# Kernel optimization log

Measured on AMD Instinct MI355X. Metric: run time of the kernel, lower is better.

## Reference

```python
import jax, jax.numpy as jnp
import numpy as np

N = 100000      # nodes
E = 1600000     # edges (before self loops)
F_IN = 128
HID = 32
H = 4
OUT = 32
NEG_SLOPE = 0.2


def setup_inputs() -> dict:
    key = jax.random.key(0)
    ks = jax.random.split(key, 10)
    x = jax.random.normal(ks[0], (N, F_IN), jnp.float32)
    edge_index = jax.random.randint(ks[1], (2, E), 0, N, jnp.int32)
    s1 = 1.0 / np.sqrt(F_IN)
    s2 = 1.0 / np.sqrt(H * HID)
    W1 = jax.random.normal(ks[2], (F_IN, H * HID), jnp.float32) * s1
    a_src1 = jax.random.normal(ks[3], (H, HID), jnp.float32) * 0.1
    a_dst1 = jax.random.normal(ks[4], (H, HID), jnp.float32) * 0.1
    b1 = jnp.zeros((H * HID,), jnp.float32)
    W2 = jax.random.normal(ks[5], (H * HID, OUT), jnp.float32) * s2
    a_src2 = jax.random.normal(ks[6], (1, OUT), jnp.float32) * 0.1
    a_dst2 = jax.random.normal(ks[7], (1, OUT), jnp.float32) * 0.1
    b2 = jnp.zeros((OUT,), jnp.float32)
    return {"x": x, "edge_index": edge_index, "W1": W1, "a_src1": a_src1,
            "a_dst1": a_dst1, "b1": b1, "W2": W2, "a_src2": a_src2,
            "a_dst2": a_dst2, "b2": b2}


def gat_conv(x, src, dst, W, a_src, a_dst, b, heads, out_ch):
    # PyG GATConv (concat=True) with self loops already appended to src/dst.
    n = x.shape[0]
    h = (x @ W).reshape(n, heads, out_ch)                 # [N,H,C]
    alpha_s = jnp.sum(h * a_src, axis=-1)                 # [N,H]
    alpha_d = jnp.sum(h * a_dst, axis=-1)                 # [N,H]
    e = jax.nn.leaky_relu(alpha_s[src] + alpha_d[dst], NEG_SLOPE)  # [E',H]
    # segment softmax over destination nodes (self loops => every segment nonempty)
    emax = jax.ops.segment_max(e, dst, num_segments=n)
    ex = jnp.exp(e - emax[dst])
    denom = jax.ops.segment_sum(ex, dst, num_segments=n)
    alpha = ex / denom[dst]                               # [E',H]
    msg = h[src] * alpha[:, :, None]                      # [E',H,C]
    out = jax.ops.segment_sum(msg, dst, num_segments=n)   # [N,H,C]
    return out.reshape(n, heads * out_ch) + b


def reference(x, edge_index, W1, a_src1, a_dst1, b1, W2, a_src2, a_dst2, b2):
    loops = jnp.arange(N, dtype=edge_index.dtype)
    src = jnp.concatenate([edge_index[0], loops])
    dst = jnp.concatenate([edge_index[1], loops])
    h = gat_conv(x, src, dst, W1, a_src1, a_dst1, b1, H, HID)
    h = jax.nn.relu(h)                                    # dropout: eval mode, no-op
    out = gat_conv(h, src, dst, W2, a_src2, a_dst2, b2, 1, OUT)
    return out
```

## Files before the change

kernel.cpp:

```cpp
#include <hip/hip_runtime.h>
#include <hip/hip_fp16.h>

#define NEG 0.2f
#define EPB 4096
#define BSH 6
#define SLOT 48
#define CAP 1280
#define KBMAX 1664

typedef _Float16 half8 __attribute__((ext_vector_type(8)));
typedef float f32x4 __attribute__((ext_vector_type(4)));

__device__ inline __half2 pun_h2(float f) { union { float f; __half2 h; } u; u.f = f; return u.h; }
__device__ inline float pun_f(__half2 h) { union { float f; __half2 h; } u; u.h = h; return u.f; }

__global__ void k_prep(const float* __restrict__ W1, const float* __restrict__ W2,
                       half8* __restrict__ Wp, half8* __restrict__ W2p,
                       int* __restrict__ gcount, int KB) {
    int b = blockIdx.x;
    if (b < 8) {
        int u = b * 256 + threadIdx.x;
        int s = u >> 9, tn = (u >> 6) & 7, lane = u & 63;
        int quad = lane >> 4, c = lane & 15;
        half8 v;
#pragma unroll
        for (int j = 0; j < 8; ++j)
            v[j] = (_Float16)W1[(s * 32 + quad * 8 + j) * 128 + tn * 16 + c];
        Wp[u] = v;
    } else if (b < 10) {
        int u = (b - 8) * 256 + threadIdx.x;
        int n = u >> 8, s = (u >> 6) & 3, lane = u & 63;
        int quad = lane >> 4, c = lane & 15;
        half8 v;
#pragma unroll
        for (int j = 0; j < 8; ++j)
            v[j] = (_Float16)W2[(s * 32 + quad * 8 + j) * 32 + n * 16 + c];
        W2p[u] = v;
    } else {
        int i = (b - 10) * 256 + threadIdx.x;
        if (i < KB) gcount[i] = 0;
    }
}

__global__ __launch_bounds__(256) void k_pA(const float* __restrict__ x,
                                            const half8* __restrict__ Wp,
                                            const float* __restrict__ a_s,
                                            const float* __restrict__ a_d,
                                            __half* __restrict__ h1h,
                                            float* __restrict__ as1,
                                            float* __restrict__ ad1, int N,
                                            const int* __restrict__ srcp,
                                            const int* __restrict__ dstp,
                                            int* __restrict__ gcount,
                                            int2* __restrict__ ebuf,
                                            int E, int KB, int ngemm) {
    __shared__ _Float16 xa[64][136];
    __shared__ int lh[KBMAX];
    int t = threadIdx.x;

    if (blockIdx.x >= ngemm) {
        int blk = blockIdx.x - ngemm;
        int base0 = blk * EPB;
        int ss[16], dd[16];
#pragma unroll
        for (int j = 0; j < 16; ++j) {
            int i = base0 + j * 256 + t;
            if (i < E) { ss[j] = srcp[i]; dd[j] = dstp[i]; } else dd[j] = -1;
        }
        for (int i = t; i < KB; i += 256) lh[i] = 0;
        __syncthreads();
#pragma unroll
        for (int j = 0; j < 16; ++j)
            if (dd[j] >= 0) atomicAdd(&lh[dd[j] >> BSH], 1);
        __syncthreads();
        for (int b = t; b < KB; b += 256) {
            int c = lh[b];
            if (c > 0) lh[b] = atomicAdd(&gcount[b], c);
        }
        __syncthreads();
#pragma unroll
        for (int j = 0; j < 16; ++j) {
            if (dd[j] >= 0) {
                int b = dd[j] >> BSH;
                int pos = atomicAdd(&lh[b], 1);
                ebuf[(size_t)b * CAP + pos] = int2{ss[j], dd[j]};
            }
        }
        return;
    }

    int row0 = blockIdx.x * 64;
    {
        int row = t >> 2;
        int col0 = (t & 3) * 32;
        int gr = row0 + row;
        const float4* xsrc = (const float4*)&x[(size_t)gr * 128 + col0];
#pragma unroll
        for (int m = 0; m < 4; ++m) {
            float4 p0, p1;
            if (gr < N) { p0 = xsrc[m * 2]; p1 = xsrc[m * 2 + 1]; }
            else { p0 = float4{0,0,0,0}; p1 = float4{0,0,0,0}; }
            _Float16* dstq = &xa[row][col0 + m * 8];
            dstq[0] = (_Float16)p0.x; dstq[1] = (_Float16)p0.y;
            dstq[2] = (_Float16)p0.z; dstq[3] = (_Float16)p0.w;
            dstq[4] = (_Float16)p1.x; dstq[5] = (_Float16)p1.y;
            dstq[6] = (_Float16)p1.z; dstq[7] = (_Float16)p1.w;
        }
    }
    __syncthreads();

    int w = t >> 6;
    int lane = t & 63;
    int quad = lane >> 4, c = lane & 15;

    f32x4 acc[8];
#pragma unroll
    for (int i = 0; i < 8; ++i) acc[i] = f32x4{0, 0, 0, 0};

#pragma unroll
    for (int s = 0; s < 4; ++s) {
        half8 a = *(const half8*)&xa[w * 16 + c][s * 32 + quad * 8];
#pragma unroll
        for (int tn = 0; tn < 8; ++tn) {
            half8 b = Wp[(s * 8 + tn) * 64 + lane];
            acc[tn] = __builtin_amdgcn_mfma_f32_16x16x32_f16(a, b, acc[tn], 0, 0, 0);
        }
    }

    float asv[8], adv[8];
#pragma unroll
    for (int tn = 0; tn < 8; ++tn) { asv[tn] = a_s[tn * 16 + c]; adv[tn] = a_d[tn * 16 + c]; }
#pragma unroll
    for (int r = 0; r < 4; ++r) {
        int gr = row0 + w * 16 + quad * 4 + r;
#pragma unroll
        for (int h = 0; h < 4; ++h) {
            float ps = acc[2*h][r] * asv[2*h] + acc[2*h+1][r] * asv[2*h+1];
            float pd = acc[2*h][r] * adv[2*h] + acc[2*h+1][r] * adv[2*h+1];
            ps += __shfl_xor(ps, 1); ps += __shfl_xor(ps, 2);
            ps += __shfl_xor(ps, 4); ps += __shfl_xor(ps, 8);
            pd += __shfl_xor(pd, 1); pd += __shfl_xor(pd, 2);
            pd += __shfl_xor(pd, 4); pd += __shfl_xor(pd, 8);
            if (c == 0 && gr < N) { as1[gr * 4 + h] = ps; ad1[gr * 4 + h] = pd; }
        }
    }

    __syncthreads();
#pragma unroll
    for (int tn = 0; tn < 8; ++tn)
#pragma unroll
        for (int r = 0; r < 4; ++r)
            xa[w * 16 + quad * 4 + r][tn * 16 + c] = (_Float16)acc[tn][r];
    __syncthreads();
    {
        int row = t >> 2;
        int seg = t & 3;
        int gr = row0 + row;
        if (gr < N) {
            float4* gp = (float4*)&h1h[(size_t)gr * 128 + seg * 32];
#pragma unroll
            for (int i = 0; i < 4; ++i)
                gp[i] = *(float4*)&xa[row][seg * 32 + i * 8];
        }
    }
}

__global__ __launch_bounds__(256) void k_aggC(const int2* __restrict__ ebuf,
                                              const int* __restrict__ gcount,
                                              const __half* __restrict__ h1h,
                                              const float* __restrict__ as1,
                                              const float* __restrict__ ad1,
                                              const float* __restrict__ b1,
                                              const half8* __restrict__ W2p,
                                              const float* __restrict__ asw,
                                              const float* __restrict__ adw,
                                              int* __restrict__ csr,
                                              int* __restrict__ counts,
                                              __half* __restrict__ h2h,
                                              float* __restrict__ as2,
                                              float* __restrict__ ad2, int N) {
    __shared__ int lcnt[64];
    __shared__ int lcsr[64 * SLOT];
    __shared__ _Float16 stg[4][16][136];
    int t = threadIdx.x;
    int b = blockIdx.x, d0 = b << BSH;

    if (t < 64) lcnt[t] = 0;
    __syncthreads();

    int ecnt = gcount[b];
    const int2* eb = &ebuf[(size_t)b * CAP];
    for (int i = t; i < ecnt; i += 256) {
        int2 e = eb[i];
        int li = e.y - d0;
        int r = atomicAdd(&lcnt[li], 1);
        lcsr[li * SLOT + r] = e.x;
    }
    __syncthreads();

    {
        int4* gc = (int4*)&csr[(size_t)d0 * SLOT];
        const int4* lc = (const int4*)lcsr;
#pragma unroll
        for (int u = 0; u < 3; ++u) gc[t + 256 * u] = lc[t + 256 * u];
        if (t < 64 && d0 + t < N) counts[d0 + t] = lcnt[t];
    }

    int w = t >> 6, lane = t & 63;
    int q = lane >> 5, c4 = lane & 31;
    int head4 = c4 >> 3;
    const __half2* hp = (const __half2*)h1h;
    float4 bv4 = *(const float4*)&b1[4 * c4];

    int quad = lane >> 4, c16 = lane & 15;
    half8 bf[2][4];
#pragma unroll
    for (int n = 0; n < 2; ++n)
#pragma unroll
        for (int s = 0; s < 4; ++s) bf[n][s] = W2p[(n * 4 + s) * 64 + lane];
    float asw0 = asw[c16], asw1 = asw[16 + c16];
    float adw0 = adw[c16], adw1 = adw[16 + c16];

    for (int i = 0; i < 16; ++i) {
        int dst = d0 + w * 16 + i;
        bool valid = dst < N;
        int li = w * 16 + i;
        int cnt = valid ? lcnt[li] : 0;
        int cbase = li * SLOT;
        float adv = valid ? ad1[dst * 4 + head4] : 0.f;
        float a0 = 0.f, a1 = 0.f, a2 = 0.f, a3 = 0.f, den = 0.f;
        if (valid && q == 0) {
            float es = as1[dst * 4 + head4] + adv;
            es = es > 0.f ? es : NEG * es;
            float xs = __expf(es);
            float2 vv = *(const float2*)&hp[(size_t)dst * 64 + 2 * c4];
            float2 f01 = __half22float2(pun_h2(vv.x));
            float2 f23 = __half22float2(pun_h2(vv.y));
            a0 = xs * f01.x; a1 = xs * f01.y; a2 = xs * f23.x; a3 = xs * f23.y;
            den = xs;
        }
        int e = q;
        for (; e + 14 < cnt; e += 16) {
            int si[8];
#pragma unroll
            for (int j = 0; j < 8; ++j) si[j] = lcsr[cbase + e + 2 * j];
            float ej[8];
#pragma unroll
            for (int j = 0; j < 8; ++j) ej[j] = as1[si[j] * 4 + head4];
            float2 vj[8];
#pragma unroll
            for (int j = 0; j < 8; ++j) vj[j] = *(const float2*)&hp[(size_t)si[j] * 64 + 2 * c4];
#pragma unroll
            for (int j = 0; j < 8; ++j) {
                float ee = ej[j] + adv;
                ee = ee > 0.f ? ee : NEG * ee;
                float xw = __expf(ee);
                float2 f01 = __half22float2(pun_h2(vj[j].x));
                float2 f23 = __half22float2(pun_h2(vj[j].y));
                a0 += xw * f01.x; a1 += xw * f01.y;
                a2 += xw * f23.x; a3 += xw * f23.y;
                den += xw;
            }
        }
        for (; e + 6 < cnt; e += 8) {
            int si[4];
#pragma unroll
            for (int j = 0; j < 4; ++j) si[j] = lcsr[cbase + e + 2 * j];
            float ej[4];
#pragma unroll
            for (int j = 0; j < 4; ++j) ej[j] = as1[si[j] * 4 + head4];
            float2 vj[4];
#pragma unroll
            for (int j = 0; j < 4; ++j) vj[j] = *(const float2*)&hp[(size_t)si[j] * 64 + 2 * c4];
#pragma unroll
            for (int j = 0; j < 4; ++j) {
                float ee = ej[j] + adv;
                ee = ee > 0.f ? ee : NEG * ee;
                float xw = __expf(ee);
                float2 f01 = __half22float2(pun_h2(vj[j].x));
                float2 f23 = __half22float2(pun_h2(vj[j].y));
                a0 += xw * f01.x; a1 += xw * f01.y;
                a2 += xw * f23.x; a3 += xw * f23.y;
                den += xw;
            }
        }
        for (; e < cnt; e += 2) {
            int s0 = lcsr[cbase + e];
            float e0v = as1[s0 * 4 + head4] + adv;
            float2 vv = *(const float2*)&hp[(size_t)s0 * 64 + 2 * c4];
            e0v = e0v > 0.f ? e0v : NEG * e0v;  float x0 = __expf(e0v);
            float2 f01 = __half22float2(pun_h2(vv.x));
            float2 f23 = __half22float2(pun_h2(vv.y));
            a0 += x0 * f01.x; a1 += x0 * f01.y;
            a2 += x0 * f23.x; a3 += x0 * f23.y;
            den += x0;
        }
        a0 += __shfl_xor(a0, 32); a1 += __shfl_xor(a1, 32);
        a2 += __shfl_xor(a2, 32); a3 += __shfl_xor(a3, 32);
        den += __shfl_xor(den, 32);
        float inv = valid ? 1.f / den : 0.f;
        float o0 = a0 * inv + bv4.x;
        float o1 = a1 * inv + bv4.y;
        float o2 = a2 * inv + bv4.z;
        float o3 = a3 * inv + bv4.w;
        o0 = o0 > 0.f ? o0 : 0.f;
        o1 = o1 > 0.f ? o1 : 0.f;
        o2 = o2 > 0.f ? o2 : 0.f;
        o3 = o3 > 0.f ? o3 : 0.f;
        if (q == 0) {
            float2 st;
            st.x = pun_f(__floats2half2_rn(o0, o1));
            st.y = pun_f(__floats2half2_rn(o2, o3));
            *(float2*)&stg[w][i][4 * c4] = st;
        }
    }

    f32x4 am0 = {0, 0, 0, 0}, am1 = {0, 0, 0, 0};
#pragma unroll
    for (int s = 0; s < 4; ++s) {
        half8 a = *(const half8*)&stg[w][c16][s * 32 + quad * 8];
        am0 = __builtin_amdgcn_mfma_f32_16x16x32_f16(a, bf[0][s], am0, 0, 0, 0);
        am1 = __builtin_amdgcn_mfma_f32_16x16x32_f16(a, bf[1][s], am1, 0, 0, 0);
    }
#pragma unroll
    for (int r = 0; r < 4; ++r) {
        int dst = d0 + w * 16 + quad * 4 + r;
        float ps = am0[r] * asw0 + am1[r] * asw1;
        float pd = am0[r] * adw0 + am1[r] * adw1;
        ps += __shfl_xor(ps, 1); ps += __shfl_xor(ps, 2);
        ps += __shfl_xor(ps, 4); ps += __shfl_xor(ps, 8);
        pd += __shfl_xor(pd, 1); pd += __shfl_xor(pd, 2);
        pd += __shfl_xor(pd, 4); pd += __shfl_xor(pd, 8);
        if (dst < N) {
            h2h[(size_t)dst * 32 + c16]      = __float2half_rn(am0[r]);
            h2h[(size_t)dst * 32 + 16 + c16] = __float2half_rn(am1[r]);
            if (c16 == 0) { as2[dst] = ps; ad2[dst] = pd; }
        }
    }
}

__global__ __launch_bounds__(256) void k_agg2(const __half* __restrict__ h2h,
                                              const float* __restrict__ as2,
                                              const float* __restrict__ ad2,
                                              const int* __restrict__ csr,
                                              const int* __restrict__ counts,
                                              const float* __restrict__ b2,
                                              float* __restrict__ out, int N) {
    int w = threadIdx.x >> 6;
    int lane = threadIdx.x & 63;
    int dst = blockIdx.x * 4 + w;
    if (dst >= N) return;
    int q = lane >> 5;
    int c = lane & 31;
    float adv = ad2[dst];
    int beg = dst * SLOT;
    int cnt = counts[dst];
    float acc = 0.f, den = 0.f;
    if (q == 0) {
        float es = as2[dst] + adv;
        es = es > 0.f ? es : NEG * es;
        float xs = __expf(es);
        acc = xs * __half2float(h2h[(size_t)dst * 32 + c]);
        den = xs;
    }
    int e = q;
    for (; e + 6 < cnt; e += 8) {
        int si[4];
#pragma unroll
        for (int j = 0; j < 4; ++j) si[j] = csr[beg + e + 2 * j];
        float ej[4];
#pragma unroll
        for (int j = 0; j < 4; ++j) ej[j] = as2[si[j]];
        float vj[4];
#pragma unroll
        for (int j = 0; j < 4; ++j) vj[j] = __half2float(h2h[(size_t)si[j] * 32 + c]);
#pragma unroll
        for (int j = 0; j < 4; ++j) {
            float ee = ej[j] + adv;
            ee = ee > 0.f ? ee : NEG * ee;
            float xw = __expf(ee);
            acc += xw * vj[j];
            den += xw;
        }
    }
    for (; e < cnt; e += 2) {
        int s0 = csr[beg + e];
        float e0 = as2[s0] + adv;
        float v0 = __half2float(h2h[(size_t)s0 * 32 + c]);
        e0 = e0 > 0.f ? e0 : NEG * e0;  float x0 = __expf(e0);
        acc += x0 * v0;
        den += x0;
    }
    acc += __shfl_xor(acc, 32, 64);
    den += __shfl_xor(den, 32, 64);
    if (q == 0) out[(size_t)dst * 32 + c] = acc / den + b2[c];
}

extern "C" void kernel_launch(void* const* d_in, const int* in_sizes, int n_in,
                              void* d_out, int out_size, void* d_ws, size_t ws_size,
                              hipStream_t stream) {
    const float* x     = (const float*)d_in[0];
    const int*   ei    = (const int*)d_in[1];
    const float* W1    = (const float*)d_in[2];
    const float* as_w1 = (const float*)d_in[3];
    const float* ad_w1 = (const float*)d_in[4];
    const float* b1    = (const float*)d_in[5];
    const float* W2    = (const float*)d_in[6];
    const float* as_w2 = (const float*)d_in[7];
    const float* ad_w2 = (const float*)d_in[8];
    const float* b2    = (const float*)d_in[9];
    float* out = (float*)d_out;

    int N  = in_sizes[0] / 128;
    int E  = in_sizes[1] / 2;
    const int* srcp = ei;
    const int* dstp = ei + E;

    int KB     = (N + 63) >> BSH;
    int ND     = KB << BSH;
    int nblkB  = (E + EPB - 1) / EPB;
    int ngemm  = (N + 63) / 64;

    char* p = (char*)d_ws;
    auto alloc = [&](size_t bytes) -> char* {
        char* r = p;
        p += (bytes + 255) & ~(size_t)255;
        return r;
    };
    __half* h1h    = (__half*)alloc((size_t)N * 128 * 2);
    float*  as1    = (float*)alloc((size_t)N * 4 * 4);
    float*  ad1    = (float*)alloc((size_t)N * 4 * 4);
    __half* h2h    = (__half*)alloc((size_t)N * 32 * 2);
    float*  as2    = (float*)alloc((size_t)N * 4);
    float*  ad2    = (float*)alloc((size_t)N * 4);
    int*    counts = (int*)alloc((size_t)ND * 4);
    int*    csr    = (int*)alloc((size_t)ND * SLOT * 4);
    half8*  Wp     = (half8*)alloc(2048 * 16);
    half8*  W2p    = (half8*)alloc(512 * 16);
    int*    gcount = (int*)alloc((size_t)KB * 4);
    int2*   ebuf   = (int2*)alloc((size_t)KB * CAP * 8);

    k_prep<<<10 + (KB + 255) / 256, 256, 0, stream>>>(W1, W2, Wp, W2p, gcount, KB);
    k_pA<<<ngemm + nblkB, 256, 0, stream>>>(x, Wp, as_w1, ad_w1, h1h, as1, ad1, N,
                                            srcp, dstp, gcount, ebuf, E, KB, ngemm);
    k_aggC<<<KB, 256, 0, stream>>>(ebuf, gcount, h1h, as1, ad1, b1,
                                   W2p, as_w2, ad_w2, csr, counts, h2h, as2, ad2, N);
    k_agg2<<<(N + 3) / 4, 256, 0, stream>>>(h2h, as2, ad2, csr, counts, b2, out, N);
}
```

Before: 291.8 us.

## Split aggC blocks into half-size 128-thread blocks and unroll agg2 gather deeper

Each 64-destination bucket is now handled by two 128-thread blocks that each scan the whole bucket edge list and keep only their 32 destinations. This halves LDS per block, adds a launch_bounds occupancy hint and defers the W2 fragment loads past the aggregation loop to reduce register pressure. In exchange every edge in a bucket is read twice. Separately, k_agg2 gains an 8-wide unrolled gather loop so more loads are in flight per iteration.

```diff
diff --git a/kernel.cpp b/kernel.cpp
--- a/kernel.cpp
+++ b/kernel.cpp
@@ -165,7 +165,7 @@
     }
 }
 
-__global__ __launch_bounds__(256) void k_aggC(const int2* __restrict__ ebuf,
+__global__ __launch_bounds__(128, 5) void k_aggC(const int2* __restrict__ ebuf,
                                               const int* __restrict__ gcount,
                                               const __half* __restrict__ h1h,
                                               const float* __restrict__ as1,
@@ -179,22 +179,26 @@
                                               __half* __restrict__ h2h,
                                               float* __restrict__ as2,
                                               float* __restrict__ ad2, int N) {
-    __shared__ int lcnt[64];
-    __shared__ int lcsr[64 * SLOT];
-    __shared__ _Float16 stg[4][16][136];
+    __shared__ int lcnt[32];
+    __shared__ int lcsr[32 * SLOT];
+    __shared__ _Float16 stg[2][16][136];
     int t = threadIdx.x;
-    int b = blockIdx.x, d0 = b << BSH;
-
-    if (t < 64) lcnt[t] = 0;
+    int b = blockIdx.x;
+    int bucket = b >> 1;
+    int d0 = b << 5;
+
+    if (t < 32) lcnt[t] = 0;
     __syncthreads();
 
-    int ecnt = gcount[b];
-    const int2* eb = &ebuf[(size_t)b * CAP];
-    for (int i = t; i < ecnt; i += 256) {
+    int ecnt = gcount[bucket];
+    const int2* eb = &ebuf[(size_t)bucket * CAP];
+    for (int i = t; i < ecnt; i += 128) {
         int2 e = eb[i];
-        int li = e.y - d0;
-        int r = atomicAdd(&lcnt[li], 1);
-        lcsr[li * SLOT + r] = e.x;
+        unsigned li = (unsigned)(e.y - d0);
+        if (li < 32u) {
+            int r = atomicAdd(&lcnt[li], 1);
+            lcsr[li * SLOT + r] = e.x;
+        }
     }
     __syncthreads();
 
@@ -202,8 +206,8 @@
         int4* gc = (int4*)&csr[(size_t)d0 * SLOT];
         const int4* lc = (const int4*)lcsr;
 #pragma unroll
-        for (int u = 0; u < 3; ++u) gc[t + 256 * u] = lc[t + 256 * u];
-        if (t < 64 && d0 + t < N) counts[d0 + t] = lcnt[t];
+        for (int u = 0; u < 3; ++u) gc[t + 128 * u] = lc[t + 128 * u];
+        if (t < 32 && d0 + t < N) counts[d0 + t] = lcnt[t];
     }
 
     int w = t >> 6, lane = t & 63;
@@ -211,15 +215,6 @@
     int head4 = c4 >> 3;
     const __half2* hp = (const __half2*)h1h;
     float4 bv4 = *(const float4*)&b1[4 * c4];
-
-    int quad = lane >> 4, c16 = lane & 15;
-    half8 bf[2][4];
-#pragma unroll
-    for (int n = 0; n < 2; ++n)
-#pragma unroll
-        for (int s = 0; s < 4; ++s) bf[n][s] = W2p[(n * 4 + s) * 64 + lane];
-    float asw0 = asw[c16], asw1 = asw[16 + c16];
-    float adw0 = adw[c16], adw1 = adw[16 + c16];
 
     for (int i = 0; i < 16; ++i) {
         int dst = d0 + w * 16 + i;
@@ -314,6 +309,15 @@
             *(float2*)&stg[w][i][4 * c4] = st;
         }
     }
+
+    int quad = lane >> 4, c16 = lane & 15;
+    half8 bf[2][4];
+#pragma unroll
+    for (int n = 0; n < 2; ++n)
+#pragma unroll
+        for (int s = 0; s < 4; ++s) bf[n][s] = W2p[(n * 4 + s) * 64 + lane];
+    float asw0 = asw[c16], asw1 = asw[16 + c16];
+    float adw0 = adw[c16], adw1 = adw[16 + c16];
 
     f32x4 am0 = {0, 0, 0, 0}, am1 = {0, 0, 0, 0};
 #pragma unroll
@@ -364,6 +368,25 @@
         den = xs;
     }
     int e = q;
+    for (; e + 14 < cnt; e += 16) {
+        int si[8];
+#pragma unroll
+        for (int j = 0; j < 8; ++j) si[j] = csr[beg + e + 2 * j];
+        float ej[8];
+#pragma unroll
+        for (int j = 0; j < 8; ++j) ej[j] = as2[si[j]];
+        float vj[8];
+#pragma unroll
+        for (int j = 0; j < 8; ++j) vj[j] = __half2float(h2h[(size_t)si[j] * 32 + c]);
+#pragma unroll
+        for (int j = 0; j < 8; ++j) {
+            float ee = ej[j] + adv;
+            ee = ee > 0.f ? ee : NEG * ee;
+            float xw = __expf(ee);
+            acc += xw * vj[j];
+            den += xw;
+        }
+    }
     for (; e + 6 < cnt; e += 8) {
         int si[4];
 #pragma unroll
@@ -443,7 +466,7 @@
     k_prep<<<10 + (KB + 255) / 256, 256, 0, stream>>>(W1, W2, Wp, W2p, gcount, KB);
     k_pA<<<ngemm + nblkB, 256, 0, stream>>>(x, Wp, as_w1, ad_w1, h1h, as1, ad1, N,
                                             srcp, dstp, gcount, ebuf, E, KB, ngemm);
-    k_aggC<<<KB, 256, 0, stream>>>(ebuf, gcount, h1h, as1, ad1, b1,
-                                   W2p, as_w2, ad_w2, csr, counts, h2h, as2, ad2, N);
+    k_aggC<<<KB * 2, 128, 0, stream>>>(ebuf, gcount, h1h, as1, ad1, b1,
+                                       W2p, as_w2, ad_w2, csr, counts, h2h, as2, ad2, N);
     k_agg2<<<(N + 3) / 4, 256, 0, stream>>>(h2h, as2, ad2, csr, counts, b2, out, N);
 }
```

After: 298.4 us. 2.3% more time.

## Aggregate layer 2 directly from bucketed edge buffer with LDS atomics, drop CSR

Applied to the files above, without the earlier changes.

k_aggC no longer writes the padded CSR and count arrays to global memory. k_agg2 now runs one block per 64-destination bucket, reads the unsorted ebuf edges directly and accumulates the softmax numerator and denominator into shared-memory arrays with atomics. The self-loop term is added in the epilogue. This removes the CSR global write and reread, and the per-node launch of 4 destinations per block, at the cost of LDS atomic contention and fewer, larger blocks. The W2 fragment loads are also moved later in k_aggC to shorten their register live range.

```diff
diff --git a/kernel.cpp b/kernel.cpp
--- a/kernel.cpp
+++ b/kernel.cpp
@@ -174,8 +174,6 @@
                                               const half8* __restrict__ W2p,
                                               const float* __restrict__ asw,
                                               const float* __restrict__ adw,
-                                              int* __restrict__ csr,
-                                              int* __restrict__ counts,
                                               __half* __restrict__ h2h,
                                               float* __restrict__ as2,
                                               float* __restrict__ ad2, int N) {
@@ -198,28 +196,11 @@
     }
     __syncthreads();
 
-    {
-        int4* gc = (int4*)&csr[(size_t)d0 * SLOT];
-        const int4* lc = (const int4*)lcsr;
-#pragma unroll
-        for (int u = 0; u < 3; ++u) gc[t + 256 * u] = lc[t + 256 * u];
-        if (t < 64 && d0 + t < N) counts[d0 + t] = lcnt[t];
-    }
-
     int w = t >> 6, lane = t & 63;
     int q = lane >> 5, c4 = lane & 31;
     int head4 = c4 >> 3;
     const __half2* hp = (const __half2*)h1h;
     float4 bv4 = *(const float4*)&b1[4 * c4];
-
-    int quad = lane >> 4, c16 = lane & 15;
-    half8 bf[2][4];
-#pragma unroll
-    for (int n = 0; n < 2; ++n)
-#pragma unroll
-        for (int s = 0; s < 4; ++s) bf[n][s] = W2p[(n * 4 + s) * 64 + lane];
-    float asw0 = asw[c16], asw1 = asw[16 + c16];
-    float adw0 = adw[c16], adw1 = adw[16 + c16];
 
     for (int i = 0; i < 16; ++i) {
         int dst = d0 + w * 16 + i;
@@ -315,6 +296,15 @@
         }
     }
 
+    int quad = lane >> 4, c16 = lane & 15;
+    half8 bf[2][4];
+#pragma unroll
+    for (int n = 0; n < 2; ++n)
+#pragma unroll
+        for (int s = 0; s < 4; ++s) bf[n][s] = W2p[(n * 4 + s) * 64 + lane];
+    float asw0 = asw[c16], asw1 = asw[16 + c16];
+    float adw0 = adw[c16], adw1 = adw[16 + c16];
+
     f32x4 am0 = {0, 0, 0, 0}, am1 = {0, 0, 0, 0};
 #pragma unroll
     for (int s = 0; s < 4; ++s) {
@@ -339,61 +329,68 @@
     }
 }
 
-__global__ __launch_bounds__(256) void k_agg2(const __half* __restrict__ h2h,
+__global__ __launch_bounds__(256) void k_agg2(const int2* __restrict__ ebuf,
+                                              const int* __restrict__ gcount,
+                                              const __half* __restrict__ h2h,
                                               const float* __restrict__ as2,
                                               const float* __restrict__ ad2,
-                                              const int* __restrict__ csr,
-                                              const int* __restrict__ counts,
                                               const float* __restrict__ b2,
                                               float* __restrict__ out, int N) {
-    int w = threadIdx.x >> 6;
-    int lane = threadIdx.x & 63;
-    int dst = blockIdx.x * 4 + w;
-    if (dst >= N) return;
-    int q = lane >> 5;
-    int c = lane & 31;
-    float adv = ad2[dst];
-    int beg = dst * SLOT;
-    int cnt = counts[dst];
-    float acc = 0.f, den = 0.f;
-    if (q == 0) {
-        float es = as2[dst] + adv;
+    __shared__ float acc[64][32];
+    __shared__ float den[64];
+    __shared__ float lad[64];
+    int t = threadIdx.x;
+    int b = blockIdx.x, d0 = b << BSH;
+
+    for (int u = t; u < 64 * 32; u += 256) ((float*)acc)[u] = 0.f;
+    if (t < 64) {
+        den[t] = 0.f;
+        lad[t] = (d0 + t < N) ? ad2[d0 + t] : 0.f;
+    }
+    __syncthreads();
+
+    int hw = t >> 5;
+    int c  = t & 31;
+    int ecnt = gcount[b];
+    const int2* eb = &ebuf[(size_t)b * CAP];
+
+    for (int base = hw * 8; base < ecnt; base += 64) {
+        int2 ed[8];
+#pragma unroll
+        for (int j = 0; j < 8; ++j)
+            if (base + j < ecnt) ed[j] = eb[base + j];
+        float asv[8];
+#pragma unroll
+        for (int j = 0; j < 8; ++j)
+            if (base + j < ecnt) asv[j] = as2[ed[j].x];
+        __half hv[8];
+#pragma unroll
+        for (int j = 0; j < 8; ++j)
+            if (base + j < ecnt) hv[j] = h2h[(size_t)ed[j].x * 32 + c];
+#pragma unroll
+        for (int j = 0; j < 8; ++j) {
+            if (base + j < ecnt) {
+                int li = ed[j].y - d0;
+                float ee = asv[j] + lad[li];
+                ee = ee > 0.f ? ee : NEG * ee;
+                float xw = __expf(ee);
+                atomicAdd(&acc[li][c], xw * __half2float(hv[j]));
+                if (c == 0) atomicAdd(&den[li], xw);
+            }
+        }
+    }
+    __syncthreads();
+
+    for (int u = t; u < 64 * 32; u += 256) {
+        int li = u >> 5, cc = u & 31;
+        int dst = d0 + li;
+        if (dst >= N) continue;
+        float es = as2[dst] + lad[li];
         es = es > 0.f ? es : NEG * es;
         float xs = __expf(es);
-        acc = xs * __half2float(h2h[(size_t)dst * 32 + c]);
-        den = xs;
-    }
-    int e = q;
-    for (; e + 6 < cnt; e += 8) {
-        int si[4];
-#pragma unroll
-        for (int j = 0; j < 4; ++j) si[j] = csr[beg + e + 2 * j];
-        float ej[4];
-#pragma unroll
-        for (int j = 0; j < 4; ++j) ej[j] = as2[si[j]];
-        float vj[4];
-#pragma unroll
-        for (int j = 0; j < 4; ++j) vj[j] = __half2float(h2h[(size_t)si[j] * 32 + c]);
-#pragma unroll
-        for (int j = 0; j < 4; ++j) {
-            float ee = ej[j] + adv;
-            ee = ee > 0.f ? ee : NEG * ee;
-            float xw = __expf(ee);
-            acc += xw * vj[j];
-            den += xw;
-        }
-    }
-    for (; e < cnt; e += 2) {
-        int s0 = csr[beg + e];
-        float e0 = as2[s0] + adv;
-        float v0 = __half2float(h2h[(size_t)s0 * 32 + c]);
-        e0 = e0 > 0.f ? e0 : NEG * e0;  float x0 = __expf(e0);
-        acc += x0 * v0;
-        den += x0;
-    }
-    acc += __shfl_xor(acc, 32, 64);
-    den += __shfl_xor(den, 32, 64);
-    if (q == 0) out[(size_t)dst * 32 + c] = acc / den + b2[c];
+        float hh = __half2float(h2h[(size_t)dst * 32 + cc]);
+        out[(size_t)dst * 32 + cc] = (acc[li][cc] + xs * hh) / (den[li] + xs) + b2[cc];
+    }
 }
 
 extern "C" void kernel_launch(void* const* d_in, const int* in_sizes, int n_in,
@@ -417,7 +414,6 @@
     const int* dstp = ei + E;
 
     int KB     = (N + 63) >> BSH;
-    int ND     = KB << BSH;
     int nblkB  = (E + EPB - 1) / EPB;
     int ngemm  = (N + 63) / 64;
 
@@ -433,8 +429,6 @@
     __half* h2h    = (__half*)alloc((size_t)N * 32 * 2);
     float*  as2    = (float*)alloc((size_t)N * 4);
     float*  ad2    = (float*)alloc((size_t)N * 4);
-    int*    counts = (int*)alloc((size_t)ND * 4);
-    int*    csr    = (int*)alloc((size_t)ND * SLOT * 4);
     half8*  Wp     = (half8*)alloc(2048 * 16);
     half8*  W2p    = (half8*)alloc(512 * 16);
     int*    gcount = (int*)alloc((size_t)KB * 4);
@@ -444,6 +438,6 @@
     k_pA<<<ngemm + nblkB, 256, 0, stream>>>(x, Wp, as_w1, ad_w1, h1h, as1, ad1, N,
                                             srcp, dstp, gcount, ebuf, E, KB, ngemm);
     k_aggC<<<KB, 256, 0, stream>>>(ebuf, gcount, h1h, as1, ad1, b1,
-                                   W2p, as_w2, ad_w2, csr, counts, h2h, as2, ad2, N);
-    k_agg2<<<(N + 3) / 4, 256, 0, stream>>>(h2h, as2, ad2, csr, counts, b2, out, N);
+                                   W2p, as_w2, ad_w2, h2h, as2, ad2, N);
+    k_agg2<<<KB, 256, 0, stream>>>(ebuf, gcount, h2h, as2, ad2, b2, out, N);
 }
```

New measurement: 551.0 us. +88.8%, slower.

## Process two destinations per wave in layer-1 aggregation and deepen layer-2 unroll

Applied to the files above, without the earlier changes.

In the fused layer-1 aggregation, each half-wave now handles its own destination node (two nodes per iteration, eight iterations) instead of both halves splitting one node's edges and then combining them with cross-lane shuffles. Each half-wave keeps two interleaved accumulator sets to preserve instruction-level parallelism, and the W2 fragment loads are moved after the loop to lower register pressure during aggregation. The layer-2 aggregation gains an 8-wide unrolled edge loop. The cost is possible load imbalance between the two half-waves when degrees differ, and more registers in layer 2.

```diff
diff --git a/kernel.cpp b/kernel.cpp
--- a/kernel.cpp
+++ b/kernel.cpp
@@ -212,24 +212,16 @@
     const __half2* hp = (const __half2*)h1h;
     float4 bv4 = *(const float4*)&b1[4 * c4];
 
-    int quad = lane >> 4, c16 = lane & 15;
-    half8 bf[2][4];
-#pragma unroll
-    for (int n = 0; n < 2; ++n)
-#pragma unroll
-        for (int s = 0; s < 4; ++s) bf[n][s] = W2p[(n * 4 + s) * 64 + lane];
-    float asw0 = asw[c16], asw1 = asw[16 + c16];
-    float adw0 = adw[c16], adw1 = adw[16 + c16];
-
-    for (int i = 0; i < 16; ++i) {
-        int dst = d0 + w * 16 + i;
+    for (int i = 0; i < 8; ++i) {
+        int li = w * 16 + 2 * i + q;
+        int dst = d0 + li;
         bool valid = dst < N;
-        int li = w * 16 + i;
         int cnt = valid ? lcnt[li] : 0;
         int cbase = li * SLOT;
         float adv = valid ? ad1[dst * 4 + head4] : 0.f;
         float a0 = 0.f, a1 = 0.f, a2 = 0.f, a3 = 0.f, den = 0.f;
-        if (valid && q == 0) {
+        float g0 = 0.f, g1 = 0.f, g2 = 0.f, g3 = 0.f, dn2 = 0.f;
+        if (valid) {
             float es = as1[dst * 4 + head4] + adv;
             es = es > 0.f ? es : NEG * es;
             float xs = __expf(es);
@@ -239,11 +231,11 @@
             a0 = xs * f01.x; a1 = xs * f01.y; a2 = xs * f23.x; a3 = xs * f23.y;
             den = xs;
         }
-        int e = q;
-        for (; e + 14 < cnt; e += 16) {
+        int e = 0;
+        for (; e + 7 < cnt; e += 8) {
             int si[8];
 #pragma unroll
-            for (int j = 0; j < 8; ++j) si[j] = lcsr[cbase + e + 2 * j];
+            for (int j = 0; j < 8; ++j) si[j] = lcsr[cbase + e + j];
             float ej[8];
 #pragma unroll
             for (int j = 0; j < 8; ++j) ej[j] = as1[si[j] * 4 + head4];
@@ -257,15 +249,21 @@
                 float xw = __expf(ee);
                 float2 f01 = __half22float2(pun_h2(vj[j].x));
                 float2 f23 = __half22float2(pun_h2(vj[j].y));
-                a0 += xw * f01.x; a1 += xw * f01.y;
-                a2 += xw * f23.x; a3 += xw * f23.y;
-                den += xw;
+                if ((j & 1) == 0) {
+                    a0 += xw * f01.x; a1 += xw * f01.y;
+                    a2 += xw * f23.x; a3 += xw * f23.y;
+                    den += xw;
+                } else {
+                    g0 += xw * f01.x; g1 += xw * f01.y;
+                    g2 += xw * f23.x; g3 += xw * f23.y;
+                    dn2 += xw;
+                }
             }
         }
-        for (; e + 6 < cnt; e += 8) {
+        for (; e + 3 < cnt; e += 4) {
             int si[4];
 #pragma unroll
-            for (int j = 0; j < 4; ++j) si[j] = lcsr[cbase + e + 2 * j];
+            for (int j = 0; j < 4; ++j) si[j] = lcsr[cbase + e + j];
             float ej[4];
 #pragma unroll
             for (int j = 0; j < 4; ++j) ej[j] = as1[si[j] * 4 + head4];
@@ -279,25 +277,29 @@
                 float xw = __expf(ee);
                 float2 f01 = __half22float2(pun_h2(vj[j].x));
                 float2 f23 = __half22float2(pun_h2(vj[j].y));
-                a0 += xw * f01.x; a1 += xw * f01.y;
-                a2 += xw * f23.x; a3 += xw * f23.y;
-                den += xw;
+                if ((j & 1) == 0) {
+                    a0 += xw * f01.x; a1 += xw * f01.y;
+                    a2 += xw * f23.x; a3 += xw * f23.y;
+                    den += xw;
+                } else {
+                    g0 += xw * f01.x; g1 += xw * f01.y;
+                    g2 += xw * f23.x; g3 += xw * f23.y;
+                    dn2 += xw;
+                }
             }
         }
-        for (; e < cnt; e += 2) {
+        for (; e < cnt; ++e) {
             int s0 = lcsr[cbase + e];
             float e0v = as1[s0 * 4 + head4] + adv;
             float2 vv = *(const float2*)&hp[(size_t)s0 * 64 + 2 * c4];
             e0v = e0v > 0.f ? e0v : NEG * e0v;  float x0 = __expf(e0v);
             float2 f01 = __half22float2(pun_h2(vv.x));
             float2 f23 = __half22float2(pun_h2(vv.y));
-            a0 += x0 * f01.x; a1 += x0 * f01.y;
-            a2 += x0 * f23.x; a3 += x0 * f23.y;
-            den += x0;
-        }
-        a0 += __shfl_xor(a0, 32); a1 += __shfl_xor(a1, 32);
-        a2 += __shfl_xor(a2, 32); a3 += __shfl_xor(a3, 32);
-        den += __shfl_xor(den, 32);
+            g0 += x0 * f01.x; g1 += x0 * f01.y;
+            g2 += x0 * f23.x; g3 += x0 * f23.y;
+            dn2 += x0;
+        }
+        a0 += g0; a1 += g1; a2 += g2; a3 += g3; den += dn2;
         float inv = valid ? 1.f / den : 0.f;
         float o0 = a0 * inv + bv4.x;
         float o1 = a1 * inv + bv4.y;
@@ -307,13 +309,20 @@
         o1 = o1 > 0.f ? o1 : 0.f;
         o2 = o2 > 0.f ? o2 : 0.f;
         o3 = o3 > 0.f ? o3 : 0.f;
-        if (q == 0) {
-            float2 st;
-            st.x = pun_f(__floats2half2_rn(o0, o1));
-            st.y = pun_f(__floats2half2_rn(o2, o3));
-            *(float2*)&stg[w][i][4 * c4] = st;
-        }
-    }
+        float2 st;
+        st.x = pun_f(__floats2half2_rn(o0, o1));
+        st.y = pun_f(__floats2half2_rn(o2, o3));
+        *(float2*)&stg[w][2 * i + q][4 * c4] = st;
+    }
+
+    int quad = lane >> 4, c16 = lane & 15;
+    half8 bf[2][4];
+#pragma unroll
+    for (int n = 0; n < 2; ++n)
+#pragma unroll
+        for (int s = 0; s < 4; ++s) bf[n][s] = W2p[(n * 4 + s) * 64 + lane];
+    float asw0 = asw[c16], asw1 = asw[16 + c16];
+    float adw0 = adw[c16], adw1 = adw[16 + c16];
 
     f32x4 am0 = {0, 0, 0, 0}, am1 = {0, 0, 0, 0};
 #pragma unroll
@@ -364,6 +373,25 @@
         den = xs;
     }
     int e = q;
+    for (; e + 14 < cnt; e += 16) {
+        int si[8];
+#pragma unroll
+        for (int j = 0; j < 8; ++j) si[j] = csr[beg + e + 2 * j];
+        float ej[8];
+#pragma unroll
+        for (int j = 0; j < 8; ++j) ej[j] = as2[si[j]];
+        float vj[8];
+#pragma unroll
+        for (int j = 0; j < 8; ++j) vj[j] = __half2float(h2h[(size_t)si[j] * 32 + c]);
+#pragma unroll
+        for (int j = 0; j < 8; ++j) {
+            float ee = ej[j] + adv;
+            ee = ee > 0.f ? ee : NEG * ee;
+            float xw = __expf(ee);
+            acc += xw * vj[j];
+            den += xw;
+        }
+    }
     for (; e + 6 < cnt; e += 8) {
         int si[4];
 #pragma unroll
```

Measured after the change: 285.6 us. 1.02x faster.
